# Performance work log

Measured on AMD Instinct MI355X. Metric: run time of the kernel, lower is better.

The kernel has to match this reference:

```python
import jax, jax.numpy as jnp
import numpy as np

H = 16
D = 1024
DH = D // H


def setup_inputs() -> dict:
    key = jax.random.key(0)
    ks = jax.random.split(key, 7)
    B, N = 4, 2048
    queries = jax.random.normal(ks[0], (B, N, D), dtype=jnp.float32)
    keys = jax.random.normal(ks[1], (B, N, D), dtype=jnp.float32)
    values = jax.random.normal(ks[2], (B, N, D), dtype=jnp.float32)
    s = 1.0 / np.sqrt(D)
    Wq = jax.random.normal(ks[3], (D, D), dtype=jnp.float32) * s
    Wk = jax.random.normal(ks[4], (D, D), dtype=jnp.float32) * s
    Wv = jax.random.normal(ks[5], (D, D), dtype=jnp.float32) * s
    Wo = jax.random.normal(ks[6], (D, D), dtype=jnp.float32) * s
    return {"queries": queries, "keys": keys, "values": values,
            "Wq": Wq, "Wk": Wk, "Wv": Wv, "Wo": Wo}


def reference(queries, keys, values, Wq, Wk, Wv, Wo):
    B, Nq, _ = queries.shape
    Nk = keys.shape[1]
    # torch Linear (no bias): y = x @ W.T
    q = (queries @ Wq.T).reshape(B, Nq, H, DH)
    k = (keys @ Wk.T).reshape(B, Nk, H, DH)
    v = (values @ Wv.T).reshape(B, Nk, H, DH)
    scale = 1.0 / jnp.sqrt(jnp.asarray(DH, dtype=q.dtype))
    scores = jnp.einsum("bqhd,bkhd->bhqk", q, k) * scale  # (B,H,Nq,Nk)
    attn = jax.nn.softmax(scores, axis=-1)
    ctx = jnp.einsum("bhqk,bkhd->bqhd", attn, v).reshape(B, Nq, D)
    return ctx @ Wo.T
```

## Files before the change

kernel.cpp:

```cpp
#include <hip/hip_runtime.h>
#include <hip/hip_bf16.h>
#include <stdint.h>

typedef short bf16x8 __attribute__((ext_vector_type(8)));
typedef float f32x4 __attribute__((ext_vector_type(4)));
typedef unsigned short u16;
typedef unsigned int u32;

#define MFMA(a, b, c) __builtin_amdgcn_mfma_f32_16x16x32_bf16(a, b, c, 0, 0, 0)

#if __has_builtin(__builtin_amdgcn_exp2f)
#define EXP2F(x) __builtin_amdgcn_exp2f(x)
#else
#define EXP2F(x) exp2f(x)
#endif
#if __has_builtin(__builtin_amdgcn_rcpf)
#define RCPF(x) __builtin_amdgcn_rcpf(x)
#else
#define RCPF(x) (1.0f / (x))
#endif

__device__ __forceinline__ u16 f2bf(float f) {
  return __builtin_bit_cast(u16, static_cast<__bf16>(f));
}

__device__ __forceinline__ bf16x8 cvt8(const float* p) {
  const float4 f0 = *(const float4*)p;
  const float4 f1 = *(const float4*)(p + 4);
  bf16x8 r;
  r[0] = (short)f2bf(f0.x); r[1] = (short)f2bf(f0.y);
  r[2] = (short)f2bf(f0.z); r[3] = (short)f2bf(f0.w);
  r[4] = (short)f2bf(f1.x); r[5] = (short)f2bf(f1.y);
  r[6] = (short)f2bf(f1.z); r[7] = (short)f2bf(f1.w);
  return r;
}

__device__ __forceinline__ void async16(const u16* g, u16* l) {
  __builtin_amdgcn_global_load_lds(
      (const __attribute__((address_space(1))) void*)g,
      (__attribute__((address_space(3))) void*)l, 16, 0, 0);
}

__global__ __launch_bounds__(256) void cvt_qk(const float* __restrict__ xq,
                                              const float* __restrict__ xk,
                                              u16* __restrict__ dq,
                                              u16* __restrict__ dk) {
  int b = (int)blockIdx.x;
  const float* s;
  u16* d;
  if (b < 4096) { s = xq; d = dq; } else { s = xk; d = dk; b -= 4096; }
  const size_t off = (size_t)b * 2048 + (size_t)threadIdx.x * 8;
  *(bf16x8*)(d + off) = cvt8(s + off);
}

__global__ __launch_bounds__(256) void cvt_vw(
    const float* __restrict__ xv, const float* __restrict__ wq,
    const float* __restrict__ wk, const float* __restrict__ wv,
    const float* __restrict__ wo, u16* __restrict__ dv, u16* __restrict__ dwq,
    u16* __restrict__ dwk, u16* __restrict__ dwv, u16* __restrict__ dwo) {
  int b = (int)blockIdx.x;
  const float* s;
  u16* d;
  if (b < 4096) { s = xv; d = dv; }
  else if (b < 4608) { s = wq; d = dwq; b -= 4096; }
  else if (b < 5120) { s = wk; d = dwk; b -= 4608; }
  else if (b < 5632) { s = wv; d = dwv; b -= 5120; }
  else { s = wo; d = dwo; b -= 5632; }
  const size_t off = (size_t)b * 2048 + (size_t)threadIdx.x * 8;
  *(bf16x8*)(d + off) = cvt8(s + off);
}

__device__ __forceinline__ void stage_gemm(const u16* __restrict__ A,
                                           const u16* __restrict__ W,
                                           u16* smA, u16* smB, int m0, int n0,
                                           int kk, int tid) {
  const int srow = tid >> 3, sblk = tid & 7;
#pragma unroll
  for (int jj = 0; jj < 4; ++jj) {
    const int row = jj * 32 + srow;
    const int sb = (sblk ^ (row & 7)) * 8;
    const int ld = (jj * 256 + tid) * 8;
    async16(A + (size_t)(m0 + row) * 1024 + kk * 64 + sb, smA + ld);
    async16(W + (size_t)(n0 + row) * 1024 + kk * 64 + sb, smB + ld);
  }
}

__device__ __forceinline__ void gemm_compute(const u16* smA, const u16* smB,
                                             f32x4 acc[4][4], int wm, int wn,
                                             int la, int q) {
#pragma unroll
  for (int ks = 0; ks < 2; ++ks) {
    bf16x8 af[4], bfr[4];
#pragma unroll
    for (int im = 0; im < 4; ++im)
      af[im] = *(const bf16x8*)(smA + (wm * 64 + im * 16 + la) * 64 +
                                (((ks * 4 + q) ^ (la & 7)) * 8));
#pragma unroll
    for (int in = 0; in < 4; ++in)
      bfr[in] = *(const bf16x8*)(smB + (wn * 64 + in * 16 + la) * 64 +
                                 (((ks * 4 + q) ^ (la & 7)) * 8));
#pragma unroll
    for (int im = 0; im < 4; ++im)
#pragma unroll
      for (int in = 0; in < 4; ++in)
        acc[im][in] = MFMA(af[im], bfr[in], acc[im][in]);
  }
}

__device__ __forceinline__ void gemm_core(const u16* __restrict__ A,
                                          const u16* __restrict__ W,
                                          u16* smA0, u16* smB0, u16* smA1,
                                          u16* smB1, f32x4 acc[4][4], int m0,
                                          int n0, int tid) {
  const int w = tid >> 6, l = tid & 63;
  const int la = l & 15, q = l >> 4;
  const int wm = w >> 1, wn = w & 1;

  stage_gemm(A, W, smA0, smB0, m0, n0, 0, tid);
  __syncthreads();
#pragma unroll 2
  for (int kk = 0; kk < 16; ++kk) {
    u16* ca = (kk & 1) ? smA1 : smA0;
    u16* cb = (kk & 1) ? smB1 : smB0;
    u16* na = (kk & 1) ? smA0 : smA1;
    u16* nb = (kk & 1) ? smB0 : smB1;
    if (kk < 15) stage_gemm(A, W, na, nb, m0, n0, kk + 1, tid);
    gemm_compute(ca, cb, acc, wm, wn, la, q);
    __syncthreads();
  }
}

__global__ __launch_bounds__(256, 2) void gemm_qkv(
    const u16* __restrict__ Xqb, const u16* __restrict__ Xkb,
    const u16* __restrict__ Xvb, const u16* __restrict__ Wqb,
    const u16* __restrict__ Wkb, const u16* __restrict__ Wvb,
    u16* __restrict__ Qh, u16* __restrict__ Kh, u16* __restrict__ VTp) {
  __shared__ u16 smA0[128 * 64], smB0[128 * 64];
  __shared__ u16 smA1[128 * 64], smB1[128 * 64];
  const int z = (int)blockIdx.z;
  const u16* A = (z == 0) ? Xqb : (z == 1) ? Xkb : Xvb;
  const u16* W = (z == 0) ? Wqb : (z == 1) ? Wkb : Wvb;
  u16* out = (z == 0) ? Qh : (z == 1) ? Kh : VTp;
  const float scale = (z == 0) ? 0.18033688011112042f : 1.0f;

  const int tid = (int)threadIdx.x;
  const int w = tid >> 6, l = tid & 63;
  const int la = l & 15, q = l >> 4;
  const int m0 = blockIdx.x * 128, n0 = blockIdx.y * 128;
  const int wm = w >> 1, wn = w & 1;

  f32x4 acc[4][4];
#pragma unroll
  for (int i = 0; i < 4; ++i)
#pragma unroll
    for (int j = 0; j < 4; ++j) acc[i][j] = (f32x4){0.f, 0.f, 0.f, 0.f};

  gemm_core(A, W, smA0, smB0, smA1, smB1, acc, m0, n0, tid);

#pragma unroll
  for (int im = 0; im < 4; ++im) {
    const int mbase = m0 + wm * 64 + im * 16 + q * 4;
#pragma unroll
    for (int in = 0; in < 4; ++in) {
      const int n = n0 + wn * 64 + in * 16 + la;
      if (z == 2) {
        const int b = mbase >> 11, nr = mbase & 2047;
        const int h = n >> 6, d = n & 63;
        uint2 val;
        val.x = (u32)f2bf(acc[im][in][0]) | ((u32)f2bf(acc[im][in][1]) << 16);
        val.y = (u32)f2bf(acc[im][in][2]) | ((u32)f2bf(acc[im][in][3]) << 16);
        *(uint2*)(VTp + ((size_t)((b * 16 + h) * 64 + d)) * 2048 + nr) = val;
      } else {
#pragma unroll
        for (int r = 0; r < 4; ++r) {
          const int mm = mbase + r;
          const int b = mm >> 11, nr = mm & 2047;
          const int h = n >> 6, d = n & 63;
          out[((size_t)((b * 16 + h) * 2048 + nr)) * 64 + d] =
              f2bf(acc[im][in][r] * scale);
        }
      }
    }
  }
}

__global__ __launch_bounds__(256, 2) void gemm_out(const u16* __restrict__ A,
                                                   const u16* __restrict__ W,
                                                   float* __restrict__ out) {
  __shared__ u16 smA0[128 * 64], smB0[128 * 64];
  __shared__ u16 smA1[128 * 64], smB1[128 * 64];
  const int tid = (int)threadIdx.x;
  const int w = tid >> 6, l = tid & 63;
  const int la = l & 15, q = l >> 4;
  const int m0 = blockIdx.x * 128, n0 = blockIdx.y * 128;
  const int wm = w >> 1, wn = w & 1;

  f32x4 acc[4][4];
#pragma unroll
  for (int i = 0; i < 4; ++i)
#pragma unroll
    for (int j = 0; j < 4; ++j) acc[i][j] = (f32x4){0.f, 0.f, 0.f, 0.f};

  gemm_core(A, W, smA0, smB0, smA1, smB1, acc, m0, n0, tid);

#pragma unroll
  for (int im = 0; im < 4; ++im) {
    const int mbase = m0 + wm * 64 + im * 16 + q * 4;
#pragma unroll
    for (int in = 0; in < 4; ++in) {
      const int n = n0 + wn * 64 + in * 16 + la;
#pragma unroll
      for (int r = 0; r < 4; ++r)
        out[(size_t)(mbase + r) * 1024 + n] = acc[im][in][r];
    }
  }
}

__global__ __launch_bounds__(256, 2) void attn_kernel(const u16* __restrict__ Qh,
                                                      const u16* __restrict__ Kh,
                                                      const u16* __restrict__ VT,
                                                      u16* __restrict__ ctx) {
  __shared__ u16 smK[128 * 64];
  __shared__ u16 smV0[64 * 128];
  __shared__ u16 smV1[64 * 128];
  __shared__ u16 smP[128 * 128];

  const int tid = (int)threadIdx.x;
  const int w = tid >> 6, l = tid & 63;
  const int la = l & 15, q = l >> 4;
  const int qt = blockIdx.x, bh = blockIdx.y;
  const u16* Qp = Qh + (size_t)bh * (2048 * 64);
  const u16* Kp = Kh + (size_t)bh * (2048 * 64);
  const u16* Vp = VT + (size_t)bh * (64 * 2048);

  bf16x8 qf[2][2];
#pragma unroll
  for (int ic = 0; ic < 2; ++ic)
#pragma unroll
    for (int ks = 0; ks < 2; ++ks)
      qf[ic][ks] = *(const bf16x8*)(Qp + (size_t)(qt * 128 + w * 32 + ic * 16 + la) * 64 +
                                    ks * 32 + q * 8);

  f32x4 accO[2][4];
#pragma unroll
  for (int ic = 0; ic < 2; ++ic)
#pragma unroll
    for (int dc = 0; dc < 4; ++dc) accO[ic][dc] = (f32x4){0.f, 0.f, 0.f, 0.f};
  float m_[2] = {-__builtin_inff(), -__builtin_inff()};
  float l_[2] = {0.f, 0.f};
  float alpha_[2];
  bool skip_[2];

  const int srow = tid >> 3, sblk = tid & 7;

  auto stageK = [&](int kt) {
#pragma unroll
    for (int jj = 0; jj < 4; ++jj) {
      const int krow = jj * 32 + srow;
      const int ksb = (sblk ^ (krow & 7)) * 8;
      async16(Kp + (size_t)(kt * 128 + krow) * 64 + ksb, smK + (jj * 256 + tid) * 8);
    }
  };
  auto stageV = [&](int kt, u16* dst) {
#pragma unroll
    for (int jj = 0; jj < 4; ++jj) {
      const int idx = jj * 256 + tid;
      const int vr = idx >> 4, vb = idx & 15;
      async16(Vp + (size_t)vr * 2048 + kt * 128 + ((vb ^ (vr & 15)) * 8),
              dst + idx * 8);
    }
  };

  stageK(0);
  stageV(0, smV0);

  for (int kt = 0; kt < 16; ++kt) {
    u16* vcur = (kt & 1) ? smV1 : smV0;
    u16* vnxt = (kt & 1) ? smV0 : smV1;
    __syncthreads();

    f32x4 st[2][8];
#pragma unroll
    for (int ic = 0; ic < 2; ++ic)
#pragma unroll
      for (int jc = 0; jc < 8; ++jc) st[ic][jc] = (f32x4){0.f, 0.f, 0.f, 0.f};
    __builtin_amdgcn_s_setprio(1);
#pragma unroll
    for (int ks = 0; ks < 2; ++ks) {
      bf16x8 kf[8];
#pragma unroll
      for (int jc = 0; jc < 8; ++jc)
        kf[jc] = *(const bf16x8*)(smK + (jc * 16 + la) * 64 +
                                  (((ks * 4 + q) ^ (la & 7)) * 8));
#pragma unroll
      for (int jc = 0; jc < 8; ++jc)
#pragma unroll
        for (int ic = 0; ic < 2; ++ic)
          st[ic][jc] = MFMA(kf[jc], qf[ic][ks], st[ic][jc]);
    }
    __builtin_amdgcn_s_setprio(0);

#pragma unroll
    for (int ic = 0; ic < 2; ++ic) {
      float mx = -__builtin_inff();
#pragma unroll
      for (int jc = 0; jc < 8; ++jc)
#pragma unroll
        for (int r = 0; r < 4; ++r) mx = fmaxf(mx, st[ic][jc][r]);
      mx = fmaxf(mx, __shfl_xor(mx, 16));
      mx = fmaxf(mx, __shfl_xor(mx, 32));
      const bool skip = (bool)__all(mx - m_[ic] <= 8.0f);
      float mnew, al;
      if (skip) { mnew = m_[ic]; al = 1.0f; }
      else { mnew = fmaxf(m_[ic], mx); al = EXP2F(m_[ic] - mnew); }
      skip_[ic] = skip;
      alpha_[ic] = al;
      float rs = 0.f;
      const int i = w * 32 + ic * 16 + la;
#pragma unroll
      for (int jc = 0; jc < 8; ++jc) {
        const float p0 = EXP2F(st[ic][jc][0] - mnew);
        const float p1 = EXP2F(st[ic][jc][1] - mnew);
        const float p2 = EXP2F(st[ic][jc][2] - mnew);
        const float p3 = EXP2F(st[ic][jc][3] - mnew);
        rs += (p0 + p1) + (p2 + p3);
        uint2 val;
        val.x = (u32)f2bf(p0) | ((u32)f2bf(p1) << 16);
        val.y = (u32)f2bf(p2) | ((u32)f2bf(p3) << 16);
        const int blk = (jc * 2 + (q >> 1)) ^ la;
        *(uint2*)(smP + i * 128 + blk * 8 + (q & 1) * 4) = val;
      }
      rs += __shfl_xor(rs, 16);
      rs += __shfl_xor(rs, 32);
      m_[ic] = mnew;
      l_[ic] = l_[ic] * alpha_[ic] + rs;
    }
    __syncthreads();

    if (kt < 15) {
      stageK(kt + 1);
      stageV(kt + 1, vnxt);
    }

#pragma unroll
    for (int ic = 0; ic < 2; ++ic)
      if (!skip_[ic]) {
#pragma unroll
        for (int r = 0; r < 4; ++r) {
          const float a = __shfl(alpha_[ic], q * 4 + r);
#pragma unroll
          for (int dc = 0; dc < 4; ++dc) accO[ic][dc][r] *= a;
        }
      }

#pragma unroll
    for (int ks = 0; ks < 4; ++ks) {
      bf16x8 pf[2], vf[4];
#pragma unroll
      for (int ic = 0; ic < 2; ++ic)
        pf[ic] = *(const bf16x8*)(smP + (w * 32 + ic * 16 + la) * 128 +
                                  (((ks * 4 + q) ^ la) * 8));
#pragma unroll
      for (int dc = 0; dc < 4; ++dc)
        vf[dc] = *(const bf16x8*)(vcur + (dc * 16 + la) * 128 +
                                  (((ks * 4 + q) ^ la) * 8));
      __builtin_amdgcn_s_setprio(1);
#pragma unroll
      for (int ic = 0; ic < 2; ++ic)
#pragma unroll
        for (int dc = 0; dc < 4; ++dc)
          accO[ic][dc] = MFMA(pf[ic], vf[dc], accO[ic][dc]);
      __builtin_amdgcn_s_setprio(0);
    }
  }

  const int b = bh >> 4, h = bh & 15;
#pragma unroll
  for (int ic = 0; ic < 2; ++ic)
#pragma unroll
    for (int r = 0; r < 4; ++r) {
      const float inv = RCPF(__shfl(l_[ic], q * 4 + r));
      const size_t rowoff =
          ((size_t)(b * 2048 + qt * 128 + w * 32 + ic * 16 + q * 4 + r)) * 1024 + h * 64;
#pragma unroll
      for (int dc = 0; dc < 4; ++dc)
        ctx[rowoff + dc * 16 + la] = f2bf(accO[ic][dc][r] * inv);
    }
}

extern "C" void kernel_launch(void* const* d_in, const int* in_sizes, int n_in,
                              void* d_out, int out_size, void* d_ws, size_t ws_size,
                              hipStream_t stream) {
  const float* Xq = (const float*)d_in[0];
  const float* Xk = (const float*)d_in[1];
  const float* Xv = (const float*)d_in[2];
  const float* Wq = (const float*)d_in[3];
  const float* Wk = (const float*)d_in[4];
  const float* Wv = (const float*)d_in[5];
  const float* Wo = (const float*)d_in[6];

  const size_t T = 8388608;
  const size_t WN = 1048576;
  u16 *Xqb, *Xkb, *Xvb, *Wqb, *Wkb, *Wvb, *Wob, *Qh, *Kh, *VTp, *ctx;
  if (ws_size >= (7 * T + 4 * WN) * sizeof(u16)) {
    u16* ws = (u16*)d_ws;
    Xqb = ws; Xkb = ws + T; Xvb = ws + 2 * T;
    Qh = ws + 3 * T; Kh = ws + 4 * T; VTp = ws + 5 * T; ctx = ws + 6 * T;
    Wqb = ws + 7 * T; Wkb = Wqb + WN; Wvb = Wkb + WN; Wob = Wvb + WN;
  } else {
    u16* ob = (u16*)d_out;
    u16* bq = (u16*)d_in[0];
    u16* bk = (u16*)d_in[1];
    u16* bv = (u16*)d_in[2];
    Xqb = ob; Xkb = ob + T;
    Xvb = bq; Wqb = bq + T; Wkb = Wqb + WN; Wvb = Wkb + WN; Wob = Wvb + WN;
    Qh = bk; Kh = bk + T;
    VTp = bv; ctx = bv + T;
  }

  dim3 blk(256);
  hipLaunchKernelGGL(cvt_qk, dim3(8192), blk, 0, stream, Xq, Xk, Xqb, Xkb);
  hipLaunchKernelGGL(cvt_vw, dim3(6144), blk, 0, stream, Xv, Wq, Wk, Wv, Wo,
                     Xvb, Wqb, Wkb, Wvb, Wob);
  hipLaunchKernelGGL(gemm_qkv, dim3(64, 8, 3), blk, 0, stream, Xqb, Xkb, Xvb,
                     Wqb, Wkb, Wvb, Qh, Kh, VTp);
  hipLaunchKernelGGL(attn_kernel, dim3(16, 64), blk, 0, stream, Qh, Kh, VTp, ctx);
  hipLaunchKernelGGL(gemm_out, dim3(64, 8), blk, 0, stream, ctx, Wob, (float*)d_out);
}
```

Measured before the change: 338.2 us.

## Enlarge QKV GEMM tile to 256x128 with 512 threads, single-buffered LDS

The QKV projection GEMM now uses 512-thread blocks (8 waves) covering a 256x128 output tile, so each staged W tile is reused across twice as many A rows. It drops the double-buffered async pipeline in favour of one LDS buffer with a sync before and after each k-step load. The intent is to cut global traffic for the weight operand and raise occupancy. The cost is that loads no longer overlap compute within a block, and the grid has half as many blocks.

```diff
diff --git a/kernel.cpp b/kernel.cpp
--- a/kernel.cpp
+++ b/kernel.cpp
@@ -70,6 +70,28 @@
   *(bf16x8*)(d + off) = cvt8(s + off);
 }
 
+__device__ __forceinline__ void gemm_compute(const u16* smA, const u16* smB,
+                                             f32x4 acc[4][4], int wm, int wn,
+                                             int la, int q) {
+#pragma unroll
+  for (int ks = 0; ks < 2; ++ks) {
+    bf16x8 af[4], bfr[4];
+#pragma unroll
+    for (int im = 0; im < 4; ++im)
+      af[im] = *(const bf16x8*)(smA + (wm * 64 + im * 16 + la) * 64 +
+                                (((ks * 4 + q) ^ (la & 7)) * 8));
+#pragma unroll
+    for (int in = 0; in < 4; ++in)
+      bfr[in] = *(const bf16x8*)(smB + (wn * 64 + in * 16 + la) * 64 +
+                                 (((ks * 4 + q) ^ (la & 7)) * 8));
+#pragma unroll
+    for (int im = 0; im < 4; ++im)
+#pragma unroll
+      for (int in = 0; in < 4; ++in)
+        acc[im][in] = MFMA(af[im], bfr[in], acc[im][in]);
+  }
+}
+
 __device__ __forceinline__ void stage_gemm(const u16* __restrict__ A,
                                            const u16* __restrict__ W,
                                            u16* smA, u16* smB, int m0, int n0,
@@ -82,28 +104,6 @@
     const int ld = (jj * 256 + tid) * 8;
     async16(A + (size_t)(m0 + row) * 1024 + kk * 64 + sb, smA + ld);
     async16(W + (size_t)(n0 + row) * 1024 + kk * 64 + sb, smB + ld);
-  }
-}
-
-__device__ __forceinline__ void gemm_compute(const u16* smA, const u16* smB,
-                                             f32x4 acc[4][4], int wm, int wn,
-                                             int la, int q) {
-#pragma unroll
-  for (int ks = 0; ks < 2; ++ks) {
-    bf16x8 af[4], bfr[4];
-#pragma unroll
-    for (int im = 0; im < 4; ++im)
-      af[im] = *(const bf16x8*)(smA + (wm * 64 + im * 16 + la) * 64 +
-                                (((ks * 4 + q) ^ (la & 7)) * 8));
-#pragma unroll
-    for (int in = 0; in < 4; ++in)
-      bfr[in] = *(const bf16x8*)(smB + (wn * 64 + in * 16 + la) * 64 +
-                                 (((ks * 4 + q) ^ (la & 7)) * 8));
-#pragma unroll
-    for (int im = 0; im < 4; ++im)
-#pragma unroll
-      for (int in = 0; in < 4; ++in)
-        acc[im][in] = MFMA(af[im], bfr[in], acc[im][in]);
   }
 }
 
@@ -130,13 +130,13 @@
   }
 }
 
-__global__ __launch_bounds__(256, 2) void gemm_qkv(
+__global__ __launch_bounds__(512, 4) void gemm_qkv(
     const u16* __restrict__ Xqb, const u16* __restrict__ Xkb,
     const u16* __restrict__ Xvb, const u16* __restrict__ Wqb,
     const u16* __restrict__ Wkb, const u16* __restrict__ Wvb,
     u16* __restrict__ Qh, u16* __restrict__ Kh, u16* __restrict__ VTp) {
-  __shared__ u16 smA0[128 * 64], smB0[128 * 64];
-  __shared__ u16 smA1[128 * 64], smB1[128 * 64];
+  __shared__ u16 smA[256 * 64];
+  __shared__ u16 smB[128 * 64];
   const int z = (int)blockIdx.z;
   const u16* A = (z == 0) ? Xqb : (z == 1) ? Xkb : Xvb;
   const u16* W = (z == 0) ? Wqb : (z == 1) ? Wkb : Wvb;
@@ -146,8 +146,9 @@
   const int tid = (int)threadIdx.x;
   const int w = tid >> 6, l = tid & 63;
   const int la = l & 15, q = l >> 4;
-  const int m0 = blockIdx.x * 128, n0 = blockIdx.y * 128;
+  const int m0 = blockIdx.x * 256, n0 = blockIdx.y * 128;
   const int wm = w >> 1, wn = w & 1;
+  const int srow = tid >> 3, sblk = tid & 7;
 
   f32x4 acc[4][4];
 #pragma unroll
@@ -155,7 +156,25 @@
 #pragma unroll
     for (int j = 0; j < 4; ++j) acc[i][j] = (f32x4){0.f, 0.f, 0.f, 0.f};
 
-  gemm_core(A, W, smA0, smB0, smA1, smB1, acc, m0, n0, tid);
+  for (int kk = 0; kk < 16; ++kk) {
+    __syncthreads();
+#pragma unroll
+    for (int jj = 0; jj < 4; ++jj) {
+      const int row = jj * 64 + srow;
+      const int sb = (sblk ^ (row & 7)) * 8;
+      async16(A + (size_t)(m0 + row) * 1024 + kk * 64 + sb,
+              smA + (jj * 512 + tid) * 8);
+    }
+#pragma unroll
+    for (int jj = 0; jj < 2; ++jj) {
+      const int row = jj * 64 + srow;
+      const int sb = (sblk ^ (row & 7)) * 8;
+      async16(W + (size_t)(n0 + row) * 1024 + kk * 64 + sb,
+              smB + (jj * 512 + tid) * 8);
+    }
+    __syncthreads();
+    gemm_compute(smA, smB, acc, wm, wn, la, q);
+  }
 
 #pragma unroll
   for (int im = 0; im < 4; ++im) {
@@ -418,12 +437,11 @@
     VTp = bv; ctx = bv + T;
   }
 
-  dim3 blk(256);
-  hipLaunchKernelGGL(cvt_qk, dim3(8192), blk, 0, stream, Xq, Xk, Xqb, Xkb);
-  hipLaunchKernelGGL(cvt_vw, dim3(6144), blk, 0, stream, Xv, Wq, Wk, Wv, Wo,
+  hipLaunchKernelGGL(cvt_qk, dim3(8192), dim3(256), 0, stream, Xq, Xk, Xqb, Xkb);
+  hipLaunchKernelGGL(cvt_vw, dim3(6144), dim3(256), 0, stream, Xv, Wq, Wk, Wv, Wo,
                      Xvb, Wqb, Wkb, Wvb, Wob);
-  hipLaunchKernelGGL(gemm_qkv, dim3(64, 8, 3), blk, 0, stream, Xqb, Xkb, Xvb,
+  hipLaunchKernelGGL(gemm_qkv, dim3(32, 8, 3), dim3(512), 0, stream, Xqb, Xkb, Xvb,
                      Wqb, Wkb, Wvb, Qh, Kh, VTp);
-  hipLaunchKernelGGL(attn_kernel, dim3(16, 64), blk, 0, stream, Qh, Kh, VTp, ctx);
-  hipLaunchKernelGGL(gemm_out, dim3(64, 8), blk, 0, stream, ctx, Wob, (float*)d_out);
-}
+  hipLaunchKernelGGL(attn_kernel, dim3(16, 64), dim3(256), 0, stream, Qh, Kh, VTp, ctx);
+  hipLaunchKernelGGL(gemm_out, dim3(64, 8), dim3(256), 0, stream, ctx, Wob, (float*)d_out);
+}
```

New measurement: 345.2 us. +2.1%, slower.
